# Kernel tuning notes

Hardware: AMD Instinct MI355X
Metric: run time of the kernel (lower is better)

## Reference

```python
import jax, jax.numpy as jnp
import numpy as np

N, E, F, H, L, K = 50000, 1200000, 64, 64, 2, 3


def setup_inputs() -> dict:
    key = jax.random.key(0)
    ks = jax.random.split(key, 12)
    return {
        "x": jax.random.normal(ks[0], (N, F), jnp.float32),
        "edge_index": jax.random.randint(ks[1], (2, E), 0, N, dtype=jnp.int32),
        "edge_weight": jax.random.uniform(ks[2], (E,), jnp.float32),
        "h": 0.1 * jax.random.normal(ks[3], (L, N, H), jnp.float32),
        "c": 0.1 * jax.random.normal(ks[4], (L, N, H), jnp.float32),
        "Wx": 0.05 * jax.random.normal(ks[5], (L, 4, H, H), jnp.float32),
        "Wcheb": 0.05 * jax.random.normal(ks[6], (L, 4, K, H, H), jnp.float32),
        "b_cheb": 0.05 * jax.random.normal(ks[7], (L, 4, H), jnp.float32),
        "w_peep": 0.05 * jax.random.normal(ks[8], (L, 3, H), jnp.float32),
        "b_gate": 0.05 * jax.random.normal(ks[9], (L, 4, H), jnp.float32),
        "fc_w": 0.05 * jax.random.normal(ks[10], (1, H), jnp.float32),
        "fc_b": jnp.zeros((1,), jnp.float32),
    }


def _cheb_basis(hl, row, col, nw, k_order):
    # Chebyshev basis T_k(L_hat) @ h. With sym normalization and lambda_max=2
    # (PyG ChebConv default), L_hat = -D^{-1/2} A D^{-1/2} with zero diagonal.
    def prop(y):  # y: (N,H) -> L_hat @ y via edge gather + scatter-add
        return jax.ops.segment_sum(nw[:, None] * y[col], row, num_segments=N)
    tx = [hl, prop(hl)]
    for _ in range(2, k_order):
        tx.append(2.0 * prop(tx[-1]) - tx[-2])
    return jnp.stack(tx, 0)  # (K, N, H)


def reference(x, edge_index, edge_weight, h, c, Wx, Wcheb, b_cheb, w_peep, b_gate, fc_w, fc_b):
    row, col = edge_index[0], edge_index[1]
    # symmetric Laplacian normalization of edge weights
    deg = jax.ops.segment_sum(edge_weight, row, num_segments=N)
    dinv = jnp.where(deg > 0, jax.lax.rsqrt(jnp.where(deg > 0, deg, 1.0)), 0.0)
    nw = -dinv[row] * edge_weight * dinv[col]  # (E,)

    inp = x
    h_new, c_new = [], []
    for l in range(L):
        hl, cl = h[l], c[l]
        tx = _cheb_basis(hl, row, col, nw, K)  # (K,N,H), shared by all 4 gate ChebConvs
        conv = jnp.einsum('knh,gkho->gno', tx, Wcheb[l]) + b_cheb[l][:, None, :]  # (4,N,H)
        gx = jnp.einsum('nf,gfo->gno', inp, Wx[l])  # (4,N,H), gate order i,f,c,o
        i = jax.nn.sigmoid(gx[0] + conv[0] + w_peep[l, 0] * cl + b_gate[l, 0])
        f = jax.nn.sigmoid(gx[1] + conv[1] + w_peep[l, 1] * cl + b_gate[l, 1])
        t = jnp.tanh(gx[2] + conv[2] + b_gate[l, 2])
        c_t = f * cl + i * t
        o = jax.nn.sigmoid(gx[3] + conv[3] + w_peep[l, 2] * c_t + b_gate[l, 3])
        h_t = o * jnp.tanh(c_t)
        h_new.append(h_t)
        c_new.append(c_t)
        inp = h_t
    out = inp @ fc_w.T + fc_b  # (N,1); dropout p=0.0 is identity
    return out, jnp.stack(h_new), jnp.stack(c_new)
```

## Files before the change

### kernel.cpp

```cpp
#include <hip/hip_runtime.h>
#include <math.h>

#define N_NODES 50000
#define E_EDGES 1200000
#define H_DIM 64
#define L_LAYERS 2
#define CSLOT 64
#define FP8_SC 16.0f
#define FP8_ISC 0.0625f

#define NB_SC 293
#define EPB   4096
#define NB_H  3125
#define NB_PK 512
#define NBKT  216
#define BKT_ROWS 232
#define SEG_CAP 56

typedef __attribute__((ext_vector_type(8))) short bf16x8;
typedef __attribute__((ext_vector_type(4))) float f32x4;
typedef __attribute__((ext_vector_type(4))) int i32x4;
typedef __attribute__((ext_vector_type(2))) unsigned int u32x2;
typedef __attribute__((ext_vector_type(4))) unsigned int u32x4;
typedef __attribute__((ext_vector_type(4))) unsigned short u16x4;

static __device__ __forceinline__ unsigned short f2bf(float f) {
    unsigned u = __float_as_uint(f);
    unsigned r = (u + 0x7FFFu + ((u >> 16) & 1u)) >> 16;
    return (unsigned short)r;
}
static __device__ __forceinline__ float bf2f(unsigned short u) {
    return __uint_as_float(((unsigned)u) << 16);
}
static __device__ __forceinline__ unsigned short pk8(float a, float b) {
    int v = __builtin_amdgcn_cvt_pk_fp8_f32(a, b, 0, false);
    return (unsigned short)(v & 0xFFFF);
}
static __device__ __forceinline__ float f8lo(unsigned u) {
    return __builtin_amdgcn_cvt_f32_fp8((int)u, 0);
}
static __device__ __forceinline__ float f8hi(unsigned u) {
    return __builtin_amdgcn_cvt_f32_fp8((int)u, 1);
}


__global__ __launch_bounds__(256) void prep_kernel(
                            const int* __restrict__ row, const int* __restrict__ col,
                            const float* __restrict__ ew,
                            u32x2* __restrict__ rec, unsigned short* __restrict__ scnt,
                            const float* __restrict__ h,
                            unsigned short* __restrict__ hbL0, unsigned short* __restrict__ hbL1,
                            const float* __restrict__ Wx, const float* __restrict__ Wcheb,
                            unsigned short* __restrict__ Wtb) {
    __shared__ int s_bcnt[NBKT];
    int b = blockIdx.x;
    int tid = threadIdx.x;
    const long NH = (long)N_NODES * H_DIM;
    if (b < NB_SC) {
        for (int i = tid; i < NBKT; i += 256) s_bcnt[i] = 0;
        __syncthreads();
        int cb = b * EPB;
        int vmax = E_EDGES / 4 - 1;
#pragma unroll
        for (int q = 0; q < 4; ++q) {
            int vb = (cb >> 2) + q * 256 + tid;
            int vi = vb > vmax ? vmax : vb;
            i32x4 rv = __builtin_nontemporal_load((const i32x4*)row + vi);
            i32x4 cv = __builtin_nontemporal_load((const i32x4*)col + vi);
            f32x4 wv = __builtin_nontemporal_load((const f32x4*)ew + vi);
            int rs[4] = {rv.x, rv.y, rv.z, rv.w};
            int cs[4] = {cv.x, cv.y, cv.z, cv.w};
            float ws[4] = {wv.x, wv.y, wv.z, wv.w};
#pragma unroll
            for (int j = 0; j < 4; ++j) {
                int e = vb * 4 + j;
                if (e < E_EDGES) {
                    int r = rs[j];
                    int g = r / BKT_ROWS;
                    int pos = atomicAdd(&s_bcnt[g], 1);
                    if (pos < SEG_CAP) {
                        u32x2 rc;
                        rc.x = (unsigned)cs[j] | ((unsigned)f2bf(ws[j]) << 16);
                        rc.y = (unsigned)r;
                        rec[((long)b * NBKT + g) * SEG_CAP + pos] = rc;
                    }
                }
            }
        }
        __syncthreads();
        for (int i = tid; i < NBKT; i += 256) {
            int c2 = s_bcnt[i]; if (c2 > SEG_CAP) c2 = SEG_CAP;
            scnt[(long)b * NBKT + i] = (unsigned short)c2;
        }
    } else if (b < NB_SC + NB_H) {
        int i = (b - NB_SC) * 256 + tid;
        f32x4 a = __builtin_nontemporal_load((const f32x4*)h + i);
        f32x4 c = __builtin_nontemporal_load((const f32x4*)(h + NH) + i);
        u16x4 o0, o1;
        o0.x = f2bf(a.x); o0.y = f2bf(a.y); o0.z = f2bf(a.z); o0.w = f2bf(a.w);
        o1.x = f2bf(c.x); o1.y = f2bf(c.y); o1.z = f2bf(c.z); o1.w = f2bf(c.w);
        __builtin_nontemporal_store(o0, (u16x4*)hbL0 + i);
        __builtin_nontemporal_store(o1, (u16x4*)hbL1 + i);
    } else {
        int i = (b - NB_SC - NB_H) * 256 + tid;
        int k = i & 255;
        int out = (i >> 8) & 255;
        int l = i >> 16;
        int g = out >> 6;
        int o = out & 63;
        float v;
        if (k < 64) {
            v = Wx[(((l * 4 + g) * 64 + k) * 64) + o];
        } else {
            int kc = (k - 64) >> 6, hh = (k - 64) & 63;
            v = Wcheb[((((l * 4 + g) * 3 + kc) * 64 + hh) * 64) + o];
        }
        __builtin_nontemporal_store(f2bf(v), Wtb + i);
    }
}


__global__ __launch_bounds__(256) void build_kernel(
    const unsigned short* __restrict__ scnt, const u32x2* __restrict__ rec,
    int* __restrict__ cnt, unsigned* __restrict__ slots4) {
    __shared__ unsigned s_slots[BKT_ROWS * CSLOT];
    __shared__ int s_cnt[BKT_ROWS];
    __shared__ unsigned short s_sc[NB_SC];
    int tid = threadIdx.x;
    int bkt = blockIdx.x;
    int rowbase = bkt * BKT_ROWS;
    int nrows = N_NODES - rowbase;
    if (nrows > BKT_ROWS) nrows = BKT_ROWS;
    if (nrows <= 0) return;

    for (int i = tid; i < BKT_ROWS; i += 256) s_cnt[i] = 0;
    for (int i = tid; i < NB_SC; i += 256) s_sc[i] = scnt[(long)i * NBKT + bkt];
    __syncthreads();

    const int TOT = NB_SC * SEG_CAP;
    for (int i = tid; i < TOT; i += 256) {
        int seg = i / SEG_CAP;
        int slot = i - seg * SEG_CAP;
        if (slot < (int)s_sc[seg]) {
            u32x2 q = rec[((long)seg * NBKT + bkt) * SEG_CAP + slot];
            int rl = (int)q.y - rowbase;
            if (rl >= 0 && rl < nrows) {
                int p = atomicAdd(&s_cnt[rl], 1);
                if (p < CSLOT) s_slots[rl * CSLOT + p] = q.x;
            }
        }
    }
    __syncthreads();

    u32x4* dst = (u32x4*)&slots4[(long)rowbase * CSLOT];
    for (int i = tid; i < nrows * (CSLOT / 4); i += 256)
        dst[i] = ((const u32x4*)s_slots)[i];
    for (int i = tid; i < nrows; i += 256) cnt[rowbase + i] = s_cnt[i];
}


__global__ __launch_bounds__(256) void rowsum_scale_kernel(
    const int* __restrict__ cnt, const unsigned* __restrict__ slots4,
    const unsigned short* __restrict__ hbL0, const unsigned short* __restrict__ hbL1,
    float* __restrict__ dinv, unsigned short* __restrict__ hb8s) {
    int lane = threadIdx.x & 63;
    int wv = threadIdx.x >> 6;
    int r = blockIdx.x * 4 + wv;
    if (r >= N_NODES) return;
    int ct = cnt[r]; if (ct > CSLOT) ct = CSLOT;
    unsigned s = slots4[(long)r * CSLOT + lane];
    float w = (lane < ct) ? bf2f((unsigned short)(s >> 16)) : 0.f;
#pragma unroll
    for (int off = 32; off >= 1; off >>= 1) w += __shfl_xor(w, off, 64);
    float dv = w > 0.f ? rsqrtf(w) : 0.f;
    if (lane == 0) dinv[r] = dv;
    long o = (long)r * 64 + lane;
    float f0 = bf2f(hbL0[o]) * dv * FP8_SC;
    float f1 = bf2f(hbL1[o]) * dv * FP8_SC;
    hb8s[o] = pk8(f0, f1);
}


__global__ __launch_bounds__(256) void spmv_f8_kernel(
    const int* __restrict__ cnt, const unsigned* __restrict__ slots4,
    const float* __restrict__ dinv,
    const unsigned short* __restrict__ y8,
    const unsigned short* __restrict__ baseL0, const unsigned short* __restrict__ baseL1,
    unsigned short* __restrict__ outL0, unsigned short* __restrict__ outL1,
    unsigned short* __restrict__ outS, int pass2) {
    __shared__ int s_col[4][64];
    __shared__ float s_w[4][64];
    int lane = threadIdx.x & 63;
    int wv = threadIdx.x >> 6;
    int r = blockIdx.x * 4 + wv;
    if (r >= N_NODES) return;
    int ct = cnt[r]; if (ct > CSLOT) ct = CSLOT;

    unsigned s = slots4[(long)r * CSLOT + lane];
    int cc = (int)(s & 0xFFFFu); if (cc >= N_NODES) cc = 0;
    s_col[wv][lane] = cc;
    s_w[wv][lane] = (lane < ct) ? bf2f((unsigned short)(s >> 16)) : 0.f;

    int ct8 = (ct + 7) & ~7;
    float a0 = 0.f, a1 = 0.f;
    for (int j = 0; j < ct8; j += 8) {
        unsigned u[8]; float w[8];
#pragma unroll
        for (int t = 0; t < 8; ++t) {
            int c = s_col[wv][j + t];
            w[t] = s_w[wv][j + t];
            u[t] = y8[(long)c * 64 + lane];
        }
#pragma unroll
        for (int t = 0; t < 8; ++t) {
            a0 += w[t] * f8lo(u[t]);
            a1 += w[t] * f8hi(u[t]);
        }
    }

    long o = (long)r * 64 + lane;
    float dr = dinv[r];
    if (!pass2) {
        float t0 = -dr * FP8_ISC * a0;
        float t1 = -dr * FP8_ISC * a1;
        outL0[o] = f2bf(t0);
        outL1[o] = f2bf(t1);
        outS[o] = pk8(FP8_SC * dr * t0, FP8_SC * dr * t1);
    } else {
        float t0 = -2.f * dr * FP8_ISC * a0 - bf2f(baseL0[o]);
        float t1 = -2.f * dr * FP8_ISC * a1 - bf2f(baseL1[o]);
        outL0[o] = f2bf(t0);
        outL1[o] = f2bf(t1);
    }
}


static __device__ __forceinline__ bf16x8 ldA(const unsigned short* const srcs[4],
                                             const float* __restrict__ xf, int use_f32,
                                             long rowoff, int k0) {
    if (use_f32 && k0 < 64) {
        const float* p = xf + rowoff + k0;
        f32x4 lo = *(const f32x4*)p;
        f32x4 hi = *(const f32x4*)(p + 4);
        bf16x8 r;
        r[0] = (short)f2bf(lo.x); r[1] = (short)f2bf(lo.y);
        r[2] = (short)f2bf(lo.z); r[3] = (short)f2bf(lo.w);
        r[4] = (short)f2bf(hi.x); r[5] = (short)f2bf(hi.y);
        r[6] = (short)f2bf(hi.z); r[7] = (short)f2bf(hi.w);
        return r;
    }
    return *(const bf16x8*)&srcs[k0 >> 6][rowoff + (k0 & 63)];
}

__global__ __launch_bounds__(512, 2) void gates_mfma_kernel(
    const float* __restrict__ inp_f,
    const unsigned short* __restrict__ s_inp,
    int use_f32,
    const unsigned short* __restrict__ s_h,
    const unsigned short* __restrict__ s_t1,
    const unsigned short* __restrict__ s_t2,
    const unsigned short* __restrict__ Wtb_l,
    const float* __restrict__ b_cheb_l, const float* __restrict__ b_gate_l,
    const float* __restrict__ w_peep_l, const float* __restrict__ cl,
    float* __restrict__ h_out, float* __restrict__ c_out,
    unsigned short* __restrict__ hob, int write_hob,
    const float* __restrict__ fcw, const float* __restrict__ fcb,
    float* __restrict__ fc_out, int do_fc) {
    __shared__ __align__(16) unsigned short s_B[256][264];

    int tid = threadIdx.x;
    int nb = blockIdx.x * 256;
    int lane = tid & 63;
    int wv = tid >> 6;
    int quad = lane >> 4;
    int l16 = lane & 15;

    {
        bf16x8 wr[8];
#pragma unroll
        for (int half = 0; half < 2; ++half) {
#pragma unroll
            for (int j = 0; j < 8; ++j) {
                int idx = tid + (half * 8 + j) * 512;
                wr[j] = *(const bf16x8*)&Wtb_l[(long)idx * 8];
            }
#pragma unroll
            for (int j = 0; j < 8; ++j) {
                int idx = tid + (half * 8 + j) * 512;
                *(bf16x8*)&s_B[idx >> 5][(idx & 31) * 8] = wr[j];
            }
        }
    }

    const unsigned short* srcs[4] = {s_inp, s_h, s_t1, s_t2};

    int nA0 = nb + wv * 32 + l16;      if (nA0 > N_NODES - 1) nA0 = N_NODES - 1;
    int nA1 = nb + wv * 32 + 16 + l16; if (nA1 > N_NODES - 1) nA1 = N_NODES - 1;
    long ro0 = (long)nA0 * 64, ro1 = (long)nA1 * 64;

    bf16x8 a0f[8], a1f[8];
#pragma unroll
    for (int j = 0; j < 3; ++j) {
        a0f[j] = ldA(srcs, inp_f, use_f32, ro0, j * 32 + quad * 8);
        a1f[j] = ldA(srcs, inp_f, use_f32, ro1, j * 32 + quad * 8);
    }

    f32x4 acc0[16], acc1[16];
#pragma unroll
    for (int nt = 0; nt < 16; ++nt) { acc0[nt] = (f32x4)(0.f); acc1[nt] = (f32x4)(0.f); }

    __syncthreads();

#pragma unroll
    for (int ks = 0; ks < 8; ++ks) {
        if (ks < 5) {
            int k0n = (ks + 3) * 32 + quad * 8;
            a0f[ks + 3] = ldA(srcs, inp_f, use_f32, ro0, k0n);
            a1f[ks + 3] = ldA(srcs, inp_f, use_f32, ro1, k0n);
        }
#pragma unroll
        for (int nt = 0; nt < 16; ++nt) {
            bf16x8 b = *(const bf16x8*)&s_B[nt * 16 + l16][ks * 32 + quad * 8];
            acc0[nt] = __builtin_amdgcn_mfma_f32_16x16x32_bf16(a0f[ks], b, acc0[nt], 0, 0, 0);
            acc1[nt] = __builtin_amdgcn_mfma_f32_16x16x32_bf16(a1f[ks], b, acc1[nt], 0, 0, 0);
        }
    }

    float bias_i[4], bias_f[4], bias_t[4], bias_o[4], wp0[4], wp1[4], wp2[4], fw[4];
#pragma unroll
    for (int oc = 0; oc < 4; ++oc) {
        int o = oc * 16 + l16;
        bias_i[oc] = b_cheb_l[0 * 64 + o] + b_gate_l[0 * 64 + o];
        bias_f[oc] = b_cheb_l[1 * 64 + o] + b_gate_l[1 * 64 + o];
        bias_t[oc] = b_cheb_l[2 * 64 + o] + b_gate_l[2 * 64 + o];
        bias_o[oc] = b_cheb_l[3 * 64 + o] + b_gate_l[3 * 64 + o];
        wp0[oc] = w_peep_l[0 * 64 + o];
        wp1[oc] = w_peep_l[1 * 64 + o];
        wp2[oc] = w_peep_l[2 * 64 + o];
        fw[oc] = do_fc ? fcw[o] : 0.f;
    }
    float fcb0 = do_fc ? fcb[0] : 0.f;

    float cv0[16], cv1[16];
#pragma unroll
    for (int r = 0; r < 4; ++r) {
#pragma unroll
        for (int oc = 0; oc < 4; ++oc) {
            int n0 = nb + wv * 32 + quad * 4 + r;      if (n0 > N_NODES - 1) n0 = N_NODES - 1;
            int n1 = nb + wv * 32 + 16 + quad * 4 + r; if (n1 > N_NODES - 1) n1 = N_NODES - 1;
            cv0[r * 4 + oc] = __builtin_nontemporal_load(cl + (long)n0 * 64 + oc * 16 + l16);
            cv1[r * 4 + oc] = __builtin_nontemporal_load(cl + (long)n1 * 64 + oc * 16 + l16);
        }
    }

#define GATE_EPILOG(ACC, CVS, MOFF)                                                   \
    _Pragma("unroll")                                                                 \
    for (int r = 0; r < 4; ++r) {                                                     \
        int n = nb + wv * 32 + (MOFF) + quad * 4 + r;                                 \
        if (n < N_NODES) {                                                            \
            float fcs = 0.f;                                                          \
            _Pragma("unroll")                                                         \
            for (int oc = 0; oc < 4; ++oc) {                                          \
                int o = oc * 16 + l16;                                                \
                long off = (long)n * 64 + o;                                          \
                float cv = CVS[r * 4 + oc];                                           \
                float gi = ACC[0 * 4 + oc][r] + bias_i[oc] + wp0[oc] * cv;            \
                float gf = ACC[1 * 4 + oc][r] + bias_f[oc] + wp1[oc] * cv;            \
                float gt = ACC[2 * 4 + oc][r] + bias_t[oc];                           \
                float go = ACC[3 * 4 + oc][r] + bias_o[oc];                           \
                float ig = 1.f / (1.f + __expf(-gi));                                 \
                float fg = 1.f / (1.f + __expf(-gf));                                 \
                float tg = tanhf(gt);                                                 \
                float ct = fg * cv + ig * tg;                                         \
                float og = 1.f / (1.f + __expf(-(go + wp2[oc] * ct)));                \
                float ht = og * tanhf(ct);                                            \
                __builtin_nontemporal_store(ht, h_out + off);                         \
                __builtin_nontemporal_store(ct, c_out + off);                         \
                if (write_hob) hob[off] = f2bf(ht);                                   \
                fcs += ht * fw[oc];                                                   \
            }                                                                         \
            if (do_fc) {                                                              \
                fcs += __shfl_xor(fcs, 1, 64);                                        \
                fcs += __shfl_xor(fcs, 2, 64);                                        \
                fcs += __shfl_xor(fcs, 4, 64);                                        \
                fcs += __shfl_xor(fcs, 8, 64);                                        \
                if (l16 == 0) fc_out[n] = fcs + fcb0;                                 \
            }                                                                         \
        }                                                                             \
    }

    GATE_EPILOG(acc0, cv0, 0)
    GATE_EPILOG(acc1, cv1, 16)
#undef GATE_EPILOG
}

extern "C" void kernel_launch(void* const* d_in, const int* in_sizes, int n_in,
                              void* d_out, int out_size, void* d_ws, size_t ws_size,
                              hipStream_t stream) {
    const float* x      = (const float*)d_in[0];
    const int*   ei     = (const int*)d_in[1];
    const float* ew     = (const float*)d_in[2];
    const float* h      = (const float*)d_in[3];
    const float* c      = (const float*)d_in[4];
    const float* Wx     = (const float*)d_in[5];
    const float* Wcheb  = (const float*)d_in[6];
    const float* b_cheb = (const float*)d_in[7];
    const float* w_peep = (const float*)d_in[8];
    const float* b_gate = (const float*)d_in[9];
    const float* fc_w   = (const float*)d_in[10];
    const float* fc_b   = (const float*)d_in[11];
    float* out = (float*)d_out;

    const int* row = ei;
    const int* col = ei + E_EDGES;
    const long NH = (long)N_NODES * H_DIM;

    float* W = (float*)d_ws;
    int*      cnt    = (int*)W;
    float*    dinv   = W + 50000;
    unsigned* slots4 = (unsigned*)(W + 100000);
    unsigned short* hbL0  = (unsigned short*)(slots4 + (long)N_NODES * CSLOT);
    unsigned short* hbL1  = hbL0 + NH;
    unsigned short* tx1L0 = hbL1 + NH;
    unsigned short* tx1L1 = tx1L0 + NH;
    unsigned short* tx2L0 = tx1L1 + NH;
    unsigned short* tx2L1 = tx2L0 + NH;
    unsigned short* hb8s  = tx2L1 + NH;
    unsigned short* t18s  = hb8s + NH;
    unsigned short* hob   = t18s + NH;
    unsigned short* Wtb   = hob + NH;
    unsigned short* scnt  = Wtb + 131072;
    u32x2* rec = (u32x2*)tx1L0;

    prep_kernel<<<NB_SC + NB_H + NB_PK, 256, 0, stream>>>(
        row, col, ew, rec, scnt, h, hbL0, hbL1, Wx, Wcheb, Wtb);
    build_kernel<<<NBKT, 256, 0, stream>>>(scnt, rec, cnt, slots4);
    rowsum_scale_kernel<<<(N_NODES + 3) / 4, 256, 0, stream>>>(cnt, slots4, hbL0, hbL1, dinv, hb8s);

    spmv_f8_kernel<<<(N_NODES + 3) / 4, 256, 0, stream>>>(
        cnt, slots4, dinv, hb8s, (const unsigned short*)nullptr, (const unsigned short*)nullptr,
        tx1L0, tx1L1, t18s, 0);
    spmv_f8_kernel<<<(N_NODES + 3) / 4, 256, 0, stream>>>(
        cnt, slots4, dinv, t18s, hbL0, hbL1,
        tx2L0, tx2L1, (unsigned short*)nullptr, 1);

    float* h_out_base = out + N_NODES;
    float* c_out_base = out + N_NODES + (long)L_LAYERS * NH;

    int gates_grid = (N_NODES + 255) / 256;

    gates_mfma_kernel<<<gates_grid, 512, 0, stream>>>(
        x, hob, 1, hbL0, tx1L0, tx2L0, Wtb,
        b_cheb, b_gate, w_peep, c,
        h_out_base, c_out_base, hob, 1,
        fc_w, fc_b, out, 0);
    gates_mfma_kernel<<<gates_grid, 512, 0, stream>>>(
        x, hob, 0, hbL1, tx1L1, tx2L1, Wtb + (long)256 * 256,
        b_cheb + 4 * 64, b_gate + 4 * 64, w_peep + 3 * 64, c + NH,
        h_out_base + NH, c_out_base + NH, hob, 0,
        fc_w, fc_b, out, 1);
}
```

Measured before the change: 296.5 us.

## Fuse rowsum into build kernel and merge both LSTM layer gate kernels

Computes degree normalization and the scaled fp8 copy of h inside the bucket build kernel, using the row slots already held in shared memory instead of rereading them in a separate launch. Merges the two per-layer gate MFMA kernels into one kernel. Each block processes layer 0, writes its hob rows, then restages weights and processes layer 1 on the same rows, prefetching layer-1 operands during the layer-0 epilogue. This removes two launches and some global traffic. The fused build runs on only 216 blocks, which may serialize the rowsum work, and the merged gates kernel carries more live registers.

```diff
diff --git a/kernel.cpp b/kernel.cpp
--- a/kernel.cpp
+++ b/kernel.cpp
@@ -122,7 +122,9 @@
 
 __global__ __launch_bounds__(256) void build_kernel(
     const unsigned short* __restrict__ scnt, const u32x2* __restrict__ rec,
-    int* __restrict__ cnt, unsigned* __restrict__ slots4) {
+    int* __restrict__ cnt, unsigned* __restrict__ slots4,
+    const unsigned short* __restrict__ hbL0, const unsigned short* __restrict__ hbL1,
+    float* __restrict__ dinv, unsigned short* __restrict__ hb8s) {
     __shared__ unsigned s_slots[BKT_ROWS * CSLOT];
     __shared__ int s_cnt[BKT_ROWS];
     __shared__ unsigned short s_sc[NB_SC];
@@ -156,28 +158,23 @@
     for (int i = tid; i < nrows * (CSLOT / 4); i += 256)
         dst[i] = ((const u32x4*)s_slots)[i];
     for (int i = tid; i < nrows; i += 256) cnt[rowbase + i] = s_cnt[i];
-}
-
-
-__global__ __launch_bounds__(256) void rowsum_scale_kernel(
-    const int* __restrict__ cnt, const unsigned* __restrict__ slots4,
-    const unsigned short* __restrict__ hbL0, const unsigned short* __restrict__ hbL1,
-    float* __restrict__ dinv, unsigned short* __restrict__ hb8s) {
-    int lane = threadIdx.x & 63;
-    int wv = threadIdx.x >> 6;
-    int r = blockIdx.x * 4 + wv;
-    if (r >= N_NODES) return;
-    int ct = cnt[r]; if (ct > CSLOT) ct = CSLOT;
-    unsigned s = slots4[(long)r * CSLOT + lane];
-    float w = (lane < ct) ? bf2f((unsigned short)(s >> 16)) : 0.f;
-#pragma unroll
-    for (int off = 32; off >= 1; off >>= 1) w += __shfl_xor(w, off, 64);
-    float dv = w > 0.f ? rsqrtf(w) : 0.f;
-    if (lane == 0) dinv[r] = dv;
-    long o = (long)r * 64 + lane;
-    float f0 = bf2f(hbL0[o]) * dv * FP8_SC;
-    float f1 = bf2f(hbL1[o]) * dv * FP8_SC;
-    hb8s[o] = pk8(f0, f1);
+
+    int lane = tid & 63;
+    int wv = tid >> 6;
+    for (int rl = wv; rl < nrows; rl += 4) {
+        int ct = s_cnt[rl]; if (ct > CSLOT) ct = CSLOT;
+        unsigned s = s_slots[rl * CSLOT + lane];
+        float w = (lane < ct) ? bf2f((unsigned short)(s >> 16)) : 0.f;
+#pragma unroll
+        for (int off = 32; off >= 1; off >>= 1) w += __shfl_xor(w, off, 64);
+        float dv = w > 0.f ? rsqrtf(w) : 0.f;
+        int r = rowbase + rl;
+        if (lane == 0) dinv[r] = dv;
+        long o = (long)r * 64 + lane;
+        float f0 = bf2f(hbL0[o]) * dv * FP8_SC;
+        float f1 = bf2f(hbL1[o]) * dv * FP8_SC;
+        hb8s[o] = pk8(f0, f1);
+    }
 }
 
 
@@ -252,22 +249,41 @@
     return *(const bf16x8*)&srcs[k0 >> 6][rowoff + (k0 & 63)];
 }
 
-__global__ __launch_bounds__(512, 2) void gates_mfma_kernel(
-    const float* __restrict__ inp_f,
-    const unsigned short* __restrict__ s_inp,
-    int use_f32,
-    const unsigned short* __restrict__ s_h,
-    const unsigned short* __restrict__ s_t1,
-    const unsigned short* __restrict__ s_t2,
-    const unsigned short* __restrict__ Wtb_l,
-    const float* __restrict__ b_cheb_l, const float* __restrict__ b_gate_l,
-    const float* __restrict__ w_peep_l, const float* __restrict__ cl,
+static __device__ __forceinline__ void stageW(const unsigned short* __restrict__ Wl,
+                                              unsigned short (*s_B)[264], int tid) {
+    bf16x8 wr[8];
+#pragma unroll
+    for (int half = 0; half < 2; ++half) {
+#pragma unroll
+        for (int j = 0; j < 8; ++j) {
+            int idx = tid + (half * 8 + j) * 512;
+            wr[j] = *(const bf16x8*)&Wl[(long)idx * 8];
+        }
+#pragma unroll
+        for (int j = 0; j < 8; ++j) {
+            int idx = tid + (half * 8 + j) * 512;
+            *(bf16x8*)&s_B[idx >> 5][(idx & 31) * 8] = wr[j];
+        }
+    }
+}
+
+__global__ __launch_bounds__(512, 2) void gates2_kernel(
+    const float* __restrict__ x,
+    unsigned short* hob,
+    const unsigned short* __restrict__ hbL0, const unsigned short* __restrict__ t1L0,
+    const unsigned short* __restrict__ t2L0,
+    const unsigned short* __restrict__ hbL1, const unsigned short* __restrict__ t1L1,
+    const unsigned short* __restrict__ t2L1,
+    const unsigned short* __restrict__ Wtb,
+    const float* __restrict__ b_cheb, const float* __restrict__ b_gate,
+    const float* __restrict__ w_peep,
+    const float* __restrict__ c_in,
     float* __restrict__ h_out, float* __restrict__ c_out,
-    unsigned short* __restrict__ hob, int write_hob,
     const float* __restrict__ fcw, const float* __restrict__ fcb,
-    float* __restrict__ fc_out, int do_fc) {
+    float* __restrict__ fc_out) {
     __shared__ __align__(16) unsigned short s_B[256][264];
 
+    const long NH = (long)N_NODES * H_DIM;
     int tid = threadIdx.x;
     int nb = blockIdx.x * 256;
     int lane = tid & 63;
@@ -275,34 +291,25 @@
     int quad = lane >> 4;
     int l16 = lane & 15;
 
-    {
-        bf16x8 wr[8];
-#pragma unroll
-        for (int half = 0; half < 2; ++half) {
-#pragma unroll
-            for (int j = 0; j < 8; ++j) {
-                int idx = tid + (half * 8 + j) * 512;
-                wr[j] = *(const bf16x8*)&Wtb_l[(long)idx * 8];
-            }
-#pragma unroll
-            for (int j = 0; j < 8; ++j) {
-                int idx = tid + (half * 8 + j) * 512;
-                *(bf16x8*)&s_B[idx >> 5][(idx & 31) * 8] = wr[j];
-            }
-        }
-    }
-
-    const unsigned short* srcs[4] = {s_inp, s_h, s_t1, s_t2};
-
     int nA0 = nb + wv * 32 + l16;      if (nA0 > N_NODES - 1) nA0 = N_NODES - 1;
     int nA1 = nb + wv * 32 + 16 + l16; if (nA1 > N_NODES - 1) nA1 = N_NODES - 1;
     long ro0 = (long)nA0 * 64, ro1 = (long)nA1 * 64;
 
+    int ne0[4], ne1[4];
+#pragma unroll
+    for (int r = 0; r < 4; ++r) {
+        ne0[r] = nb + wv * 32 + quad * 4 + r;
+        ne1[r] = nb + wv * 32 + 16 + quad * 4 + r;
+    }
+
+    stageW(Wtb, s_B, tid);
+
+    const unsigned short* srcs0[4] = {hob , hbL0, t1L0, t2L0};
     bf16x8 a0f[8], a1f[8];
 #pragma unroll
     for (int j = 0; j < 3; ++j) {
-        a0f[j] = ldA(srcs, inp_f, use_f32, ro0, j * 32 + quad * 8);
-        a1f[j] = ldA(srcs, inp_f, use_f32, ro1, j * 32 + quad * 8);
+        a0f[j] = ldA(srcs0, x, 1, ro0, j * 32 + quad * 8);
+        a1f[j] = ldA(srcs0, x, 1, ro1, j * 32 + quad * 8);
     }
 
     f32x4 acc0[16], acc1[16];
@@ -315,8 +322,8 @@
     for (int ks = 0; ks < 8; ++ks) {
         if (ks < 5) {
             int k0n = (ks + 3) * 32 + quad * 8;
-            a0f[ks + 3] = ldA(srcs, inp_f, use_f32, ro0, k0n);
-            a1f[ks + 3] = ldA(srcs, inp_f, use_f32, ro1, k0n);
+            a0f[ks + 3] = ldA(srcs0, x, 1, ro0, k0n);
+            a1f[ks + 3] = ldA(srcs0, x, 1, ro1, k0n);
         }
 #pragma unroll
         for (int nt = 0; nt < 16; ++nt) {
@@ -326,72 +333,160 @@
         }
     }
 
-    float bias_i[4], bias_f[4], bias_t[4], bias_o[4], wp0[4], wp1[4], wp2[4], fw[4];
-#pragma unroll
-    for (int oc = 0; oc < 4; ++oc) {
-        int o = oc * 16 + l16;
-        bias_i[oc] = b_cheb_l[0 * 64 + o] + b_gate_l[0 * 64 + o];
-        bias_f[oc] = b_cheb_l[1 * 64 + o] + b_gate_l[1 * 64 + o];
-        bias_t[oc] = b_cheb_l[2 * 64 + o] + b_gate_l[2 * 64 + o];
-        bias_o[oc] = b_cheb_l[3 * 64 + o] + b_gate_l[3 * 64 + o];
-        wp0[oc] = w_peep_l[0 * 64 + o];
-        wp1[oc] = w_peep_l[1 * 64 + o];
-        wp2[oc] = w_peep_l[2 * 64 + o];
-        fw[oc] = do_fc ? fcw[o] : 0.f;
-    }
-    float fcb0 = do_fc ? fcb[0] : 0.f;
-
-    float cv0[16], cv1[16];
-#pragma unroll
-    for (int r = 0; r < 4; ++r) {
+    __syncthreads();
+
+    stageW(Wtb + (long)256 * 256, s_B, tid);
+
+    const unsigned short* srcs1[4] = {hob, hbL1, t1L1, t2L1};
+    bf16x8 b0f[8], b1f[8];
+#pragma unroll
+    for (int j = 2; j < 5; ++j) {
+        b0f[j] = ldA(srcs1, x, 0, ro0, j * 32 + quad * 8);
+        b1f[j] = ldA(srcs1, x, 0, ro1, j * 32 + quad * 8);
+    }
+
+    {
+        float bias_i[4], bias_f[4], bias_t[4], bias_o[4], wp0[4], wp1[4], wp2[4];
 #pragma unroll
         for (int oc = 0; oc < 4; ++oc) {
-            int n0 = nb + wv * 32 + quad * 4 + r;      if (n0 > N_NODES - 1) n0 = N_NODES - 1;
-            int n1 = nb + wv * 32 + 16 + quad * 4 + r; if (n1 > N_NODES - 1) n1 = N_NODES - 1;
-            cv0[r * 4 + oc] = __builtin_nontemporal_load(cl + (long)n0 * 64 + oc * 16 + l16);
-            cv1[r * 4 + oc] = __builtin_nontemporal_load(cl + (long)n1 * 64 + oc * 16 + l16);
-        }
-    }
-
-#define GATE_EPILOG(ACC, CVS, MOFF)                                                   \
-    _Pragma("unroll")                                                                 \
-    for (int r = 0; r < 4; ++r) {                                                     \
-        int n = nb + wv * 32 + (MOFF) + quad * 4 + r;                                 \
-        if (n < N_NODES) {                                                            \
-            float fcs = 0.f;                                                          \
-            _Pragma("unroll")                                                         \
-            for (int oc = 0; oc < 4; ++oc) {                                          \
-                int o = oc * 16 + l16;                                                \
-                long off = (long)n * 64 + o;                                          \
-                float cv = CVS[r * 4 + oc];                                           \
-                float gi = ACC[0 * 4 + oc][r] + bias_i[oc] + wp0[oc] * cv;            \
-                float gf = ACC[1 * 4 + oc][r] + bias_f[oc] + wp1[oc] * cv;            \
-                float gt = ACC[2 * 4 + oc][r] + bias_t[oc];                           \
-                float go = ACC[3 * 4 + oc][r] + bias_o[oc];                           \
-                float ig = 1.f / (1.f + __expf(-gi));                                 \
-                float fg = 1.f / (1.f + __expf(-gf));                                 \
-                float tg = tanhf(gt);                                                 \
-                float ct = fg * cv + ig * tg;                                         \
-                float og = 1.f / (1.f + __expf(-(go + wp2[oc] * ct)));                \
-                float ht = og * tanhf(ct);                                            \
-                __builtin_nontemporal_store(ht, h_out + off);                         \
-                __builtin_nontemporal_store(ct, c_out + off);                         \
-                if (write_hob) hob[off] = f2bf(ht);                                   \
-                fcs += ht * fw[oc];                                                   \
+            int o = oc * 16 + l16;
+            bias_i[oc] = b_cheb[0 * 64 + o] + b_gate[0 * 64 + o];
+            bias_f[oc] = b_cheb[1 * 64 + o] + b_gate[1 * 64 + o];
+            bias_t[oc] = b_cheb[2 * 64 + o] + b_gate[2 * 64 + o];
+            bias_o[oc] = b_cheb[3 * 64 + o] + b_gate[3 * 64 + o];
+            wp0[oc] = w_peep[0 * 64 + o];
+            wp1[oc] = w_peep[1 * 64 + o];
+            wp2[oc] = w_peep[2 * 64 + o];
+        }
+        float cv0[16], cv1[16];
+#pragma unroll
+        for (int r = 0; r < 4; ++r)
+#pragma unroll
+            for (int oc = 0; oc < 4; ++oc) {
+                int n0 = ne0[r] > N_NODES - 1 ? N_NODES - 1 : ne0[r];
+                int n1 = ne1[r] > N_NODES - 1 ? N_NODES - 1 : ne1[r];
+                cv0[r * 4 + oc] = __builtin_nontemporal_load(c_in + (long)n0 * 64 + oc * 16 + l16);
+                cv1[r * 4 + oc] = __builtin_nontemporal_load(c_in + (long)n1 * 64 + oc * 16 + l16);
+            }
+
+#define EPILOG0(ACC, CVS, NE)                                                         \
+        _Pragma("unroll")                                                             \
+        for (int r = 0; r < 4; ++r) {                                                 \
+            int n = NE[r];                                                            \
+            if (n < N_NODES) {                                                        \
+                _Pragma("unroll")                                                     \
+                for (int oc = 0; oc < 4; ++oc) {                                      \
+                    int o = oc * 16 + l16;                                            \
+                    long off = (long)n * 64 + o;                                      \
+                    float cv = CVS[r * 4 + oc];                                       \
+                    float gi = ACC[0 * 4 + oc][r] + bias_i[oc] + wp0[oc] * cv;        \
+                    float gf = ACC[1 * 4 + oc][r] + bias_f[oc] + wp1[oc] * cv;        \
+                    float gt = ACC[2 * 4 + oc][r] + bias_t[oc];                       \
+                    float go = ACC[3 * 4 + oc][r] + bias_o[oc];                       \
+                    float ig = 1.f / (1.f + __expf(-gi));                             \
+                    float fg = 1.f / (1.f + __expf(-gf));                             \
+                    float tg = tanhf(gt);                                             \
+                    float ct = fg * cv + ig * tg;                                     \
+                    float og = 1.f / (1.f + __expf(-(go + wp2[oc] * ct)));            \
+                    float ht = og * tanhf(ct);                                        \
+                    __builtin_nontemporal_store(ht, h_out + off);                     \
+                    __builtin_nontemporal_store(ct, c_out + off);                     \
+                    hob[off] = f2bf(ht);     \
+                }                                                                     \
             }                                                                         \
-            if (do_fc) {                                                              \
+        }
+        EPILOG0(acc0, cv0, ne0)
+        EPILOG0(acc1, cv1, ne1)
+#undef EPILOG0
+    }
+
+    __syncthreads();
+
+#pragma unroll
+    for (int j = 0; j < 2; ++j) {
+        b0f[j] = ldA(srcs1, x, 0, ro0, j * 32 + quad * 8);
+        b1f[j] = ldA(srcs1, x, 0, ro1, j * 32 + quad * 8);
+    }
+#pragma unroll
+    for (int nt = 0; nt < 16; ++nt) { acc0[nt] = (f32x4)(0.f); acc1[nt] = (f32x4)(0.f); }
+
+#pragma unroll
+    for (int ks = 0; ks < 8; ++ks) {
+        if (ks >= 2 && ks < 5) {
+            int k0n = (ks + 3) * 32 + quad * 8;
+            b0f[ks + 3] = ldA(srcs1, x, 0, ro0, k0n);
+            b1f[ks + 3] = ldA(srcs1, x, 0, ro1, k0n);
+        }
+#pragma unroll
+        for (int nt = 0; nt < 16; ++nt) {
+            bf16x8 b = *(const bf16x8*)&s_B[nt * 16 + l16][ks * 32 + quad * 8];
+            acc0[nt] = __builtin_amdgcn_mfma_f32_16x16x32_bf16(b0f[ks], b, acc0[nt], 0, 0, 0);
+            acc1[nt] = __builtin_amdgcn_mfma_f32_16x16x32_bf16(b1f[ks], b, acc1[nt], 0, 0, 0);
+        }
+    }
+
+    {
+        float bias_i[4], bias_f[4], bias_t[4], bias_o[4], wp0[4], wp1[4], wp2[4], fw[4];
+#pragma unroll
+        for (int oc = 0; oc < 4; ++oc) {
+            int o = oc * 16 + l16;
+            bias_i[oc] = b_cheb[4 * 64 + 0 * 64 + o] + b_gate[4 * 64 + 0 * 64 + o];
+            bias_f[oc] = b_cheb[4 * 64 + 1 * 64 + o] + b_gate[4 * 64 + 1 * 64 + o];
+            bias_t[oc] = b_cheb[4 * 64 + 2 * 64 + o] + b_gate[4 * 64 + 2 * 64 + o];
+            bias_o[oc] = b_cheb[4 * 64 + 3 * 64 + o] + b_gate[4 * 64 + 3 * 64 + o];
+            wp0[oc] = w_peep[3 * 64 + 0 * 64 + o];
+            wp1[oc] = w_peep[3 * 64 + 1 * 64 + o];
+            wp2[oc] = w_peep[3 * 64 + 2 * 64 + o];
+            fw[oc] = fcw[o];
+        }
+        float fcb0 = fcb[0];
+        float cv0[16], cv1[16];
+#pragma unroll
+        for (int r = 0; r < 4; ++r)
+#pragma unroll
+            for (int oc = 0; oc < 4; ++oc) {
+                int n0 = ne0[r] > N_NODES - 1 ? N_NODES - 1 : ne0[r];
+                int n1 = ne1[r] > N_NODES - 1 ? N_NODES - 1 : ne1[r];
+                cv0[r * 4 + oc] = __builtin_nontemporal_load(c_in + NH + (long)n0 * 64 + oc * 16 + l16);
+                cv1[r * 4 + oc] = __builtin_nontemporal_load(c_in + NH + (long)n1 * 64 + oc * 16 + l16);
+            }
+
+#define EPILOG1(ACC, CVS, NE)                                                         \
+        _Pragma("unroll")                                                             \
+        for (int r = 0; r < 4; ++r) {                                                 \
+            int n = NE[r];                                                            \
+            if (n < N_NODES) {                                                        \
+                float fcs = 0.f;                                                      \
+                _Pragma("unroll")                                                     \
+                for (int oc = 0; oc < 4; ++oc) {                                      \
+                    int o = oc * 16 + l16;                                            \
+                    long off = NH + (long)n * 64 + o;                                 \
+                    float cv = CVS[r * 4 + oc];                                       \
+                    float gi = ACC[0 * 4 + oc][r] + bias_i[oc] + wp0[oc] * cv;        \
+                    float gf = ACC[1 * 4 + oc][r] + bias_f[oc] + wp1[oc] * cv;        \
+                    float gt = ACC[2 * 4 + oc][r] + bias_t[oc];                       \
+                    float go = ACC[3 * 4 + oc][r] + bias_o[oc];                       \
+                    float ig = 1.f / (1.f + __expf(-gi));                             \
+                    float fg = 1.f / (1.f + __expf(-gf));                             \
+                    float tg = tanhf(gt);                                             \
+                    float ct = fg * cv + ig * tg;                                     \
+                    float og = 1.f / (1.f + __expf(-(go + wp2[oc] * ct)));            \
+                    float ht = og * tanhf(ct);                                        \
+                    __builtin_nontemporal_store(ht, h_out + off);                     \
+                    __builtin_nontemporal_store(ct, c_out + off);                     \
+                    fcs += ht * fw[oc];                                               \
+                }                                                                     \
                 fcs += __shfl_xor(fcs, 1, 64);                                        \
                 fcs += __shfl_xor(fcs, 2, 64);                                        \
                 fcs += __shfl_xor(fcs, 4, 64);                                        \
                 fcs += __shfl_xor(fcs, 8, 64);                                        \
                 if (l16 == 0) fc_out[n] = fcs + fcb0;                                 \
             }                                                                         \
-        }                                                                             \
-    }
-
-    GATE_EPILOG(acc0, cv0, 0)
-    GATE_EPILOG(acc1, cv1, 16)
-#undef GATE_EPILOG
+        }
+        EPILOG1(acc0, cv0, ne0)
+        EPILOG1(acc1, cv1, ne1)
+#undef EPILOG1
+    }
 }
 
 extern "C" void kernel_launch(void* const* d_in, const int* in_sizes, int n_in,
@@ -434,8 +529,7 @@
 
     prep_kernel<<<NB_SC + NB_H + NB_PK, 256, 0, stream>>>(
         row, col, ew, rec, scnt, h, hbL0, hbL1, Wx, Wcheb, Wtb);
-    build_kernel<<<NBKT, 256, 0, stream>>>(scnt, rec, cnt, slots4);
-    rowsum_scale_kernel<<<(N_NODES + 3) / 4, 256, 0, stream>>>(cnt, slots4, hbL0, hbL1, dinv, hb8s);
+    build_kernel<<<NBKT, 256, 0, stream>>>(scnt, rec, cnt, slots4, hbL0, hbL1, dinv, hb8s);
 
     spmv_f8_kernel<<<(N_NODES + 3) / 4, 256, 0, stream>>>(
         cnt, slots4, dinv, hb8s, (const unsigned short*)nullptr, (const unsigned short*)nullptr,
@@ -449,14 +543,11 @@
 
     int gates_grid = (N_NODES + 255) / 256;
 
-    gates_mfma_kernel<<<gates_grid, 512, 0, stream>>>(
-        x, hob, 1, hbL0, tx1L0, tx2L0, Wtb,
-        b_cheb, b_gate, w_peep, c,
-        h_out_base, c_out_base, hob, 1,
-        fc_w, fc_b, out, 0);
-    gates_mfma_kernel<<<gates_grid, 512, 0, stream>>>(
-        x, hob, 0, hbL1, tx1L1, tx2L1, Wtb + (long)256 * 256,
-        b_cheb + 4 * 64, b_gate + 4 * 64, w_peep + 3 * 64, c + NH,
-        h_out_base + NH, c_out_base + NH, hob, 0,
-        fc_w, fc_b, out, 1);
-}
+    gates2_kernel<<<gates_grid, 512, 0, stream>>>(
+        x, hob,
+        hbL0, tx1L0, tx2L0,
+        hbL1, tx1L1, tx2L1,
+        Wtb, b_cheb, b_gate, w_peep,
+        c, h_out_base, c_out_base,
+        fc_w, fc_b, out);
+}
```

After: 340.6 us. 14.9% more time.
